# Kernel tuning notes

Hardware: AMD Instinct MI355X
Metric: run time of the kernel (lower is better)

The kernel has to match this reference:

```python
import jax, jax.numpy as jnp
import numpy as np

N, C, E = 4096, 128, 10          # nodes, channels, element types
LMAX = 2
NI = (LMAX + 1) ** 2             # 9 spherical components of node_feats
K = {1: 4, 2: 12, 3: 30}         # number of CG paths per correlation order
DIMS = [2 * L + 1 for L in range(LMAX + 1)]  # output irrep dims [1,3,5]


def setup_inputs() -> dict:
    key = jax.random.key(0)
    ks = iter(jax.random.split(key, 64))
    inp = {}
    inp["node_feats"] = jax.random.normal(next(ks), (N, C, NI), jnp.float32)
    inp["sc"] = jax.random.normal(next(ks), (N, C * sum(DIMS)), jnp.float32)
    z = jax.random.randint(next(ks), (N,), 0, E)
    inp["node_attrs"] = jax.nn.one_hot(z, E, dtype=jnp.float32)
    for L, d in enumerate(DIMS):
        # U tensors: fixed Clebsch-Gordan-structured constants (stand-in values,
        # correct shapes/contraction pattern of MACE's U_matrix buffers).
        inp[f"U3_L{L}"] = jax.random.normal(next(ks), (d, NI, NI, NI, K[3]), jnp.float32) * 0.05
        inp[f"U2_L{L}"] = jax.random.normal(next(ks), (d, NI, NI, K[2]), jnp.float32) * 0.05
        inp[f"U1_L{L}"] = jax.random.normal(next(ks), (d, NI, K[1]), jnp.float32) * 0.05
        # Element-dependent path weights [num_elements, k, channels]
        inp[f"W3_L{L}"] = jax.random.normal(next(ks), (E, K[3], C), jnp.float32) / np.sqrt(K[3])
        inp[f"W2_L{L}"] = jax.random.normal(next(ks), (E, K[2], C), jnp.float32) / np.sqrt(K[2])
        inp[f"W1_L{L}"] = jax.random.normal(next(ks), (E, K[1], C), jnp.float32) / np.sqrt(K[1])
        # o3.Linear channel-mixing weight for this irrep
        inp[f"lin_L{L}"] = jax.random.normal(next(ks), (C, C), jnp.float32)
    return inp


def _contract(x, y, U3, U2, U1, W3, W2, W1):
    """MACE symmetric contraction (correlation=3) for one output irrep.
    x: [b,c,n] node feats, y: [b,e] one-hot element attrs.
    Recursive einsum structure from mace.modules.symmetric_contraction.Contraction."""
    out = jnp.einsum('dijnk,ekc,bcn,be->bcdij', U3, W3, x, y)
    c2 = jnp.einsum('dijk,ekc,be->bcdij', U2, W2, y) + out
    out = jnp.einsum('bcdij,bcj->bcdi', c2, x)
    c1 = jnp.einsum('dik,ekc,be->bcdi', U1, W1, y) + out
    return jnp.einsum('bcdi,bci->bcd', c1, x)  # [b,c,d]


def reference(node_feats, sc, node_attrs,
              U3_L0, U2_L0, U1_L0, W3_L0, W2_L0, W1_L0, lin_L0,
              U3_L1, U2_L1, U1_L1, W3_L1, W2_L1, W1_L1, lin_L1,
              U3_L2, U2_L2, U1_L2, W3_L2, W2_L2, W1_L2, lin_L2):
    Us = [(U3_L0, U2_L0, U1_L0), (U3_L1, U2_L1, U1_L1), (U3_L2, U2_L2, U1_L2)]
    Ws = [(W3_L0, W2_L0, W1_L0), (W3_L1, W2_L1, W1_L1), (W3_L2, W2_L2, W1_L2)]
    lins = [lin_L0, lin_L1, lin_L2]
    c = node_feats.shape[1]
    norm = jnp.asarray(1.0 / np.sqrt(c), node_feats.dtype)
    outs = []
    for (u3, u2, u1), (w3, w2, w1), lw in zip(Us, Ws, lins):
        o = _contract(node_feats, node_attrs, u3, u2, u1, w3, w2, w1)  # [b,c,d]
        o = jnp.einsum('bcd,cf->bfd', o, lw) * norm                    # o3.Linear mix
        outs.append(o.reshape(o.shape[0], -1))
    return jnp.concatenate(outs, axis=-1) + sc
```

## Files before the change

kernel.cpp:

```cpp
#include <hip/hip_runtime.h>

#define NNODES 4096
#define NCH    128
#define NE     10
#define PADN   4736
#define NCHUNK 74
#define TSTRIDE 2048
#define DGSTRIDE 672


struct MTab { unsigned short v[220]; };
static constexpr MTab make_mtab() {
    MTab t{};
    int m = 0;
    for (int i = 0; i < 9; ++i) {
        t.v[m++] = (unsigned short)((1 << 12) | (i << 8) | (i << 4) | i);
        for (int j = i; j < 9; ++j) {
            t.v[m++] = (unsigned short)((2 << 12) | (i << 8) | (j << 4) | j);
            for (int n = j; n < 9; ++n)
                t.v[m++] = (unsigned short)((3 << 12) | (i << 8) | (j << 4) | n);
        }
    }
    return t;
}
__constant__ MTab c_mtab = make_mtab();

__device__ __forceinline__ float dot30(const float* __restrict__ U3, int dloc, int row,
                                       const float (&w3)[30])
{
    const float2* u = (const float2*)(U3 + ((size_t)dloc * 729 + row) * 30);
    float v = 0.0f;
#pragma unroll
    for (int kk = 0; kk < 15; ++kk) {
        float2 a = u[kk];
        v = fmaf(a.x, w3[2 * kk], v);
        v = fmaf(a.y, w3[2 * kk + 1], v);
    }
    return v;
}

__global__ __launch_bounds__(256) void k_pre(
    const float* __restrict__ attrs,
    const float* __restrict__ U3_0, const float* __restrict__ U3_1, const float* __restrict__ U3_2,
    const float* __restrict__ W3_0, const float* __restrict__ W3_1, const float* __restrict__ W3_2,
    const float* __restrict__ U2_0, const float* __restrict__ U2_1, const float* __restrict__ U2_2,
    const float* __restrict__ W2_0, const float* __restrict__ W2_1, const float* __restrict__ W2_2,
    const float* __restrict__ U1_0, const float* __restrict__ U1_1, const float* __restrict__ U1_2,
    const float* __restrict__ W1_0, const float* __restrict__ W1_1, const float* __restrict__ W1_2,
    float* __restrict__ Sws, int* __restrict__ list, int* __restrict__ chunkinfo)
{
    __shared__ __align__(16) float tile[32 * 129];
    int bid = blockIdx.x, t = threadIdx.x;
    if (bid < 630) {
        int e = bid / 63, r = bid - e * 63;
        int D = r / 7, chunk0 = (r - D * 7) * 32;
        int c = t & 127, sub = t >> 7;
        const float *U3, *U2, *U1, *W3, *W2, *W1; int dloc;
        if (D == 0)      { U3 = U3_0; U2 = U2_0; U1 = U1_0; W3 = W3_0; W2 = W2_0; W1 = W1_0; dloc = 0; }
        else if (D < 4)  { U3 = U3_1; U2 = U2_1; U1 = U1_1; W3 = W3_1; W2 = W2_1; W1 = W1_1; dloc = D - 1; }
        else             { U3 = U3_2; U2 = U2_2; U1 = U1_2; W3 = W3_2; W2 = W2_2; W1 = W1_2; dloc = D - 4; }
        float w3[30], w2[12], w1[4];
#pragma unroll
        for (int k = 0; k < 30; ++k) w3[k] = W3[((size_t)e * 30 + k) * 128 + c];
#pragma unroll
        for (int k = 0; k < 12; ++k) w2[k] = W2[((size_t)e * 12 + k) * 128 + c];
#pragma unroll
        for (int k = 0; k < 4; ++k)  w1[k] = W1[((size_t)e * 4 + k) * 128 + c];
#pragma unroll 1
        for (int rr = sub * 16; rr < sub * 16 + 16; ++rr) {
            int m = chunk0 + rr;
            float val = 0.0f;
            if (m < 219) {
                unsigned mv = c_mtab.v[m];
                int kind = mv >> 12, i = (mv >> 8) & 15, j = (mv >> 4) & 15, n = mv & 15;
                if (kind == 1) {
                    const float* u = U1 + (size_t)(dloc * 9 + i) * 4;
#pragma unroll
                    for (int k = 0; k < 4; ++k) val = fmaf(u[k], w1[k], val);
                } else if (kind == 2) {
                    const float* ua = U2 + (size_t)(dloc * 81 + i * 9 + j) * 12;
#pragma unroll
                    for (int k = 0; k < 12; ++k) val = fmaf(ua[k], w2[k], val);
                    if (i != j) {
                        const float* ub = U2 + (size_t)(dloc * 81 + j * 9 + i) * 12;
#pragma unroll
                        for (int k = 0; k < 12; ++k) val = fmaf(ub[k], w2[k], val);
                    }
                } else {
                    int r1 = -1, r2 = -1, r3 = -1, r4 = -1, r5 = -1;
                    if (i == j) {
                        if (j != n) { r1 = i * 81 + n * 9 + i; r2 = n * 81 + i * 9 + i; }
                    } else if (j == n) {
                        r1 = j * 81 + i * 9 + j; r2 = j * 81 + j * 9 + i;
                    } else {
                        r1 = i * 81 + n * 9 + j; r2 = j * 81 + i * 9 + n;
                        r3 = j * 81 + n * 9 + i; r4 = n * 81 + i * 9 + j;
                        r5 = n * 81 + j * 9 + i;
                    }
                    val = dot30(U3, dloc, i * 81 + j * 9 + n, w3);
                    if (r1 >= 0) { val += dot30(U3, dloc, r1, w3); val += dot30(U3, dloc, r2, w3); }
                    if (r3 >= 0) {
                        val += dot30(U3, dloc, r3, w3); val += dot30(U3, dloc, r4, w3);
                        val += dot30(U3, dloc, r5, w3);
                    }
                }
            }
            tile[rr * 129 + c] = val;
        }
        __syncthreads();
        int dg = D / 3, dr = D - dg * 3;
#pragma unroll 1
        for (int wv = 0; wv < 16; ++wv) {
            int idx = t + 256 * wv;
            int cc = idx >> 5, rr = idx & 31;
            int m = chunk0 + rr;
            if (m < 219)
                Sws[((size_t)e * 128 + cc) * TSTRIDE + dg * DGSTRIDE + m * 3 + dr] = tile[rr * 129 + cc];
        }
    } else {
        __shared__ int hist[NE], cur[NE], base[NE + 1], cbase[NE + 1];
        if (t < NE) { hist[t] = 0; cur[t] = 0; }
        __syncthreads();
        int mye[16];
#pragma unroll
        for (int k = 0; k < 16; ++k) {
            int b = k * 256 + t;
            const float* y = attrs + (size_t)b * NE;
            int e = 0;
#pragma unroll
            for (int u = 0; u < NE; ++u) if (y[u] > 0.5f) e = u;
            mye[k] = e;
            atomicAdd(&hist[e], 1);
        }
        for (int i = t; i < PADN; i += 256) list[i] = -1;
        __syncthreads();
        if (t == 0) {
            int off = 0, goff = 0;
            for (int e = 0; e < NE; ++e) {
                base[e] = off; cbase[e] = goff;
                int nc = (hist[e] + 63) >> 6;
                off += nc * 64; goff += nc;
            }
            base[NE] = off; cbase[NE] = goff;
        }
        __syncthreads();
        if (t < 80) {
            int info = -1;
            if (t < cbase[NE]) {
                int e = 0;
                while (!(t >= cbase[e] && t < cbase[e + 1])) ++e;
                int k = t - cbase[e];
                int valid = hist[e] - k * 64; if (valid > 64) valid = 64;
                info = (base[e] + k * 64) | (valid << 16) | (e << 24);
            }
            chunkinfo[t] = info;
        }
#pragma unroll
        for (int k = 0; k < 16; ++k) {
            int e = mye[k];
            int pos = atomicAdd(&cur[e], 1);
            list[base[e] + pos] = k * 256 + t;
        }
    }
}

__global__ __launch_bounds__(256) void k_gather(
    const float* __restrict__ nf, const int* __restrict__ list, float* __restrict__ xg)
{
    __shared__ __align__(16) float smem[64 * 73];
    __shared__ int lb[64];
    int qb = blockIdx.x >> 4, ct = blockIdx.x & 15;
    int c0 = ct * 8;
    int t = threadIdx.x;
    if (t < 64) lb[t] = list[qb * 64 + t];
    __syncthreads();
#pragma unroll 1
    for (int k = 0; k < 18; ++k) {
        int idx = k * 256 + t;
        int node = idx / 72, elem = idx - node * 72;
        int nb = lb[node];
        float v = 0.0f;
        if (nb >= 0) v = nf[(size_t)nb * 1152 + c0 * 9 + elem];
        smem[node * 73 + elem] = v;
    }
    __syncthreads();
#pragma unroll 1
    for (int k = 0; k < 18; ++k) {
        int idx = k * 256 + t;
        int node = idx & 63, re = idx >> 6;
        xg[((size_t)(c0 * 9 + re)) * PADN + qb * 64 + node] = smem[node * 73 + re];
    }
}

__global__ __launch_bounds__(256) void k_main(
    const float* __restrict__ xg, const int* __restrict__ chunkinfo,
    const float* __restrict__ Sws, float* __restrict__ pre)
{
    __shared__ __align__(16) float tabs[4][TSTRIDE];
    int c = blockIdx.x;
    int w = threadIdx.x >> 6, lane = threadIdx.x & 63;
    int g = blockIdx.y * 4 + w;
    int info = __builtin_amdgcn_readfirstlane(chunkinfo[g]);
    if (info == -1) return;
    int beg = info & 0xffff;
    int e = (info >> 24) & 0xff;
    int pos = beg + lane;

    {
        const float4* src = (const float4*)(Sws + ((size_t)e * NCH + c) * TSTRIDE);
        float4* dst = (float4*)tabs[w];
#pragma unroll
        for (int k = 0; k < 8; ++k)
            dst[lane + k * 64] = src[lane + k * 64];
    }

    const float* xq = xg + (size_t)c * 9 * PADN;
    float* prep     = pre + (size_t)c * 9 * PADN;

    float x[9];
#pragma unroll
    for (int n = 0; n < 9; ++n) x[n] = xq[(size_t)n * PADN + pos];

#pragma unroll 1
    for (int dg = 0; dg < 3; ++dg) {
        const float* s = tabs[w] + dg * DGSTRIDE;
        float a3[3] = {0.0f, 0.0f, 0.0f};
        int p = 0;
#pragma unroll
        for (int i = 0; i < 9; ++i) {
            float a2[3];
#pragma unroll
            for (int d = 0; d < 3; ++d) a2[d] = s[p + d];
            p += 3;
#pragma unroll
            for (int j = i; j < 9; ++j) {
                float a1[3];
#pragma unroll
                for (int d = 0; d < 3; ++d) a1[d] = s[p + d];
                p += 3;
#pragma unroll
                for (int n = j; n < 9; ++n) {
#pragma unroll
                    for (int d = 0; d < 3; ++d) a1[d] = fmaf(s[p + d], x[n], a1[d]);
                    p += 3;
                }
#pragma unroll
                for (int d = 0; d < 3; ++d) a2[d] = fmaf(a1[d], x[j], a2[d]);
            }
#pragma unroll
            for (int d = 0; d < 3; ++d) a3[d] = fmaf(a2[d], x[i], a3[d]);
        }
#pragma unroll
        for (int d = 0; d < 3; ++d)
            prep[(size_t)(dg * 3 + d) * PADN + pos] = a3[d];
    }
}

__global__ __launch_bounds__(256) void k_mixout(
    const float* __restrict__ pre, const int* __restrict__ list,
    const int* __restrict__ chunkinfo, const float* __restrict__ sc,
    const float* __restrict__ lin0, const float* __restrict__ lin1,
    const float* __restrict__ lin2, float* __restrict__ out)
{
    __shared__ __align__(16) float pt[128 * 64];
    int g = blockIdx.x, D = blockIdx.y;
    if (chunkinfo[g] == -1) return;
    int t = threadIdx.x;

    {
        int q4 = (t & 15) * 4;
        int cb = t >> 4;
#pragma unroll
        for (int k = 0; k < 8; ++k) {
            int c = cb + k * 16;
            float4 v = *(const float4*)&pre[((size_t)c * 9 + D) * PADN + g * 64 + q4];
            *(float4*)&pt[c * 64 + q4] = v;
        }
    }
    __syncthreads();

    int tq = t & 63;
    int f0 = __builtin_amdgcn_readfirstlane(t >> 6) * 32;
    int q = g * 64 + tq;
    const float* lin; int L, dl;
    if (D == 0)      { lin = lin0; L = 0; dl = 0; }
    else if (D < 4)  { lin = lin1; L = 1; dl = D - 1; }
    else             { lin = lin2; L = 2; dl = D - 4; }

    float acc[32];
#pragma unroll
    for (int f = 0; f < 32; ++f) acc[f] = 0.0f;

#pragma unroll 4
    for (int c = 0; c < 128; ++c) {
        float pv = pt[c * 64 + tq];
        const float* lr = lin + c * 128 + f0;
#pragma unroll
        for (int f = 0; f < 32; ++f)
            acc[f] = fmaf(pv, lr[f], acc[f]);
    }

    int b = list[q];
    if (b < 0) return;
    const float nrm = 0.08838834764831845f;
    const float* scb = sc + (size_t)b * 1152;
    float* ob = out + (size_t)b * 1152;
    if (L == 0) {
#pragma unroll
        for (int f = 0; f < 32; ++f)
            ob[f0 + f] = fmaf(nrm, acc[f], scb[f0 + f]);
    } else if (L == 1) {
#pragma unroll
        for (int f = 0; f < 32; ++f) {
            int col = 128 + (f0 + f) * 3 + dl;
            ob[col] = fmaf(nrm, acc[f], scb[col]);
        }
    } else {
#pragma unroll
        for (int f = 0; f < 32; ++f) {
            int col = 512 + (f0 + f) * 5 + dl;
            ob[col] = fmaf(nrm, acc[f], scb[col]);
        }
    }
}

extern "C" void kernel_launch(void* const* d_in, const int* in_sizes, int n_in,
                              void* d_out, int out_size, void* d_ws, size_t ws_size,
                              hipStream_t stream)
{
    const float* nf    = (const float*)d_in[0];
    const float* sc    = (const float*)d_in[1];
    const float* attrs = (const float*)d_in[2];
    const float *U3s[3], *U2s[3], *U1s[3], *W3s[3], *W2s[3], *W1s[3], *lins[3];
    for (int L = 0; L < 3; ++L) {
        const int o = 3 + 7 * L;
        U3s[L]  = (const float*)d_in[o + 0];
        U2s[L]  = (const float*)d_in[o + 1];
        U1s[L]  = (const float*)d_in[o + 2];
        W3s[L]  = (const float*)d_in[o + 3];
        W2s[L]  = (const float*)d_in[o + 4];
        W1s[L]  = (const float*)d_in[o + 5];
        lins[L] = (const float*)d_in[o + 6];
    }

    float* wsf     = (float*)d_ws;
    int* chunkinfo = (int*)d_ws;
    int* list      = chunkinfo + 80;
    float* Sws = wsf + 4864;
    float* pre = Sws + (size_t)NE * NCH * TSTRIDE;
    float* xg  = pre + (size_t)NCH * 9 * PADN;

    k_pre<<<631, 256, 0, stream>>>(attrs,
                                   U3s[0], U3s[1], U3s[2], W3s[0], W3s[1], W3s[2],
                                   U2s[0], U2s[1], U2s[2], W2s[0], W2s[1], W2s[2],
                                   U1s[0], U1s[1], U1s[2], W1s[0], W1s[1], W1s[2],
                                   Sws, list, chunkinfo);
    k_gather<<<1184, 256, 0, stream>>>(nf, list, xg);
    k_main<<<dim3(128, 19), 256, 0, stream>>>(xg, chunkinfo, Sws, pre);
    k_mixout<<<dim3(NCHUNK, 9), 256, 0, stream>>>(pre, list, chunkinfo, sc,
                                                  lins[0], lins[1], lins[2], (float*)d_out);
}
```

Measured before the change: 294.4 us.

## Split mix/output into two kernels with coalesced scatter; aggregate histogram atomics

Splits the fused channel-mix and output-scatter into two kernels. k_mix computes the linear mix into an intermediate buffer (reusing the gather workspace) with more blocks and fewer accumulators per thread. k_out then transposes tiles through shared memory so each node's output row is written contiguously with sc added, replacing the strided per-column global stores. The node-bucketing in k_pre also switches from one shared atomic per node to wave-level ballot aggregation. This adds an extra launch and a round trip through global memory for the mixed values.

New measurement: 435.0 us. 1.48x slower.

```diff
diff --git a/kernel.cpp b/kernel.cpp
--- a/kernel.cpp
+++ b/kernel.cpp
@@ -119,6 +119,8 @@
         }
     } else {
         __shared__ int hist[NE], cur[NE], base[NE + 1], cbase[NE + 1];
+        int lane = t & 63;
+        unsigned long long lmask = (1ull << lane) - 1ull;
         if (t < NE) { hist[t] = 0; cur[t] = 0; }
         __syncthreads();
         int mye[16];
@@ -130,7 +132,12 @@
 #pragma unroll
             for (int u = 0; u < NE; ++u) if (y[u] > 0.5f) e = u;
             mye[k] = e;
-            atomicAdd(&hist[e], 1);
+#pragma unroll
+            for (int u = 0; u < NE; ++u) {
+                unsigned long long m = __ballot(e == u);
+                if (m != 0ull && lane == (__ffsll((long long)m) - 1))
+                    atomicAdd(&hist[u], __popcll(m));
+            }
         }
         for (int i = t; i < PADN; i += 256) list[i] = -1;
         __syncthreads();
@@ -158,8 +165,18 @@
 #pragma unroll
         for (int k = 0; k < 16; ++k) {
             int e = mye[k];
-            int pos = atomicAdd(&cur[e], 1);
-            list[base[e] + pos] = k * 256 + t;
+#pragma unroll
+            for (int u = 0; u < NE; ++u) {
+                unsigned long long m = __ballot(e == u);
+                if (m != 0ull) {
+                    int leader = __ffsll((long long)m) - 1;
+                    int bs = 0;
+                    if (lane == leader) bs = atomicAdd(&cur[u], __popcll(m));
+                    bs = __shfl(bs, leader);
+                    if (e == u)
+                        list[base[u] + bs + __popcll(m & lmask)] = k * 256 + t;
+                }
+            }
         }
     }
 }
@@ -256,15 +273,20 @@
     }
 }
 
-__global__ __launch_bounds__(256) void k_mixout(
-    const float* __restrict__ pre, const int* __restrict__ list,
-    const int* __restrict__ chunkinfo, const float* __restrict__ sc,
+__global__ __launch_bounds__(256) void k_mix(
+    const float* __restrict__ pre, const int* __restrict__ chunkinfo,
     const float* __restrict__ lin0, const float* __restrict__ lin1,
-    const float* __restrict__ lin2, float* __restrict__ out)
+    const float* __restrict__ lin2, float* __restrict__ mixed)
 {
     __shared__ __align__(16) float pt[128 * 64];
-    int g = blockIdx.x, D = blockIdx.y;
+    int bid = blockIdx.x;
+    int nt = bid >> 1;
+    int fbase = (bid & 1) * 64;
+    int n0 = nt * 64;
+    int D = nt / NCHUNK;
+    int g = nt - D * NCHUNK;
     if (chunkinfo[g] == -1) return;
+    const float* lin = (D == 0) ? lin0 : (D < 4 ? lin1 : lin2);
     int t = threadIdx.x;
 
     {
@@ -273,54 +295,67 @@
 #pragma unroll
         for (int k = 0; k < 8; ++k) {
             int c = cb + k * 16;
-            float4 v = *(const float4*)&pre[((size_t)c * 9 + D) * PADN + g * 64 + q4];
+            float4 v = *(const float4*)&pre[(size_t)c * 9 * PADN + n0 + q4];
             *(float4*)&pt[c * 64 + q4] = v;
         }
     }
     __syncthreads();
 
     int tq = t & 63;
-    int f0 = __builtin_amdgcn_readfirstlane(t >> 6) * 32;
-    int q = g * 64 + tq;
-    const float* lin; int L, dl;
-    if (D == 0)      { lin = lin0; L = 0; dl = 0; }
-    else if (D < 4)  { lin = lin1; L = 1; dl = D - 1; }
-    else             { lin = lin2; L = 2; dl = D - 4; }
-
-    float acc[32];
-#pragma unroll
-    for (int f = 0; f < 32; ++f) acc[f] = 0.0f;
+    int f0 = fbase + __builtin_amdgcn_readfirstlane(t >> 6) * 16;
+    float acc[16];
+#pragma unroll
+    for (int f = 0; f < 16; ++f) acc[f] = 0.0f;
 
 #pragma unroll 4
     for (int c = 0; c < 128; ++c) {
         float pv = pt[c * 64 + tq];
         const float* lr = lin + c * 128 + f0;
 #pragma unroll
-        for (int f = 0; f < 32; ++f)
+        for (int f = 0; f < 16; ++f)
             acc[f] = fmaf(pv, lr[f], acc[f]);
     }
 
-    int b = list[q];
-    if (b < 0) return;
     const float nrm = 0.08838834764831845f;
-    const float* scb = sc + (size_t)b * 1152;
-    float* ob = out + (size_t)b * 1152;
-    if (L == 0) {
-#pragma unroll
-        for (int f = 0; f < 32; ++f)
-            ob[f0 + f] = fmaf(nrm, acc[f], scb[f0 + f]);
-    } else if (L == 1) {
-#pragma unroll
-        for (int f = 0; f < 32; ++f) {
-            int col = 128 + (f0 + f) * 3 + dl;
-            ob[col] = fmaf(nrm, acc[f], scb[col]);
-        }
-    } else {
-#pragma unroll
-        for (int f = 0; f < 32; ++f) {
-            int col = 512 + (f0 + f) * 5 + dl;
-            ob[col] = fmaf(nrm, acc[f], scb[col]);
-        }
+#pragma unroll
+    for (int f = 0; f < 16; ++f)
+        mixed[(size_t)(f0 + f) * 9 * PADN + n0 + tq] = acc[f] * nrm;
+}
+
+__global__ __launch_bounds__(256) void k_out(
+    const float* __restrict__ mixed, const int* __restrict__ list,
+    const int* __restrict__ chunkinfo, const float* __restrict__ sc,
+    float* __restrict__ out)
+{
+    __shared__ float tr[64 * 73];
+    int fc = blockIdx.x, g = blockIdx.y;
+    if (chunkinfo[g] == -1) return;
+    int t = threadIdx.x;
+    int fbase = fc * 8;
+    int tf = t >> 6, tq = t & 63;
+
+#pragma unroll
+    for (int k = 0; k < 18; ++k) {
+        int row = k * 4 + tf;
+        int f = row / 9, D = row - f * 9;
+        float v = mixed[((size_t)(fbase + f) * 9 + D) * PADN + g * 64 + tq];
+        tr[tq * 73 + row] = v;
+    }
+    __syncthreads();
+
+#pragma unroll 1
+    for (int k = 0; k < 18; ++k) {
+        int idx = k * 256 + t;
+        int node = idx / 72, col = idx - node * 72;
+        int b = list[g * 64 + node];
+        if (b < 0) continue;
+        int row, gcol;
+        if (col < 8)       { row = col * 9;                       gcol = fbase + col; }
+        else if (col < 32) { int u = col - 8;  int f = u / 3, dl = u - f * 3;
+                             row = f * 9 + 1 + dl;                gcol = 128 + fbase * 3 + u; }
+        else               { int u = col - 32; int f = u / 5, dl = u - f * 5;
+                             row = f * 9 + 4 + dl;                gcol = 512 + fbase * 5 + u; }
+        out[(size_t)b * 1152 + gcol] = tr[node * 73 + row] + sc[(size_t)b * 1152 + gcol];
     }
 }
 
@@ -349,6 +384,7 @@
     float* Sws = wsf + 4864;
     float* pre = Sws + (size_t)NE * NCH * TSTRIDE;
     float* xg  = pre + (size_t)NCH * 9 * PADN;
+    float* mixed = xg;
 
     k_pre<<<631, 256, 0, stream>>>(attrs,
                                    U3s[0], U3s[1], U3s[2], W3s[0], W3s[1], W3s[2],
@@ -357,6 +393,6 @@
                                    Sws, list, chunkinfo);
     k_gather<<<1184, 256, 0, stream>>>(nf, list, xg);
     k_main<<<dim3(128, 19), 256, 0, stream>>>(xg, chunkinfo, Sws, pre);
-    k_mixout<<<dim3(NCHUNK, 9), 256, 0, stream>>>(pre, list, chunkinfo, sc,
-                                                  lins[0], lins[1], lins[2], (float*)d_out);
-}
+    k_mix<<<1332, 256, 0, stream>>>(pre, chunkinfo, lins[0], lins[1], lins[2], mixed);
+    k_out<<<dim3(16, NCHUNK), 256, 0, stream>>>(mixed, list, chunkinfo, sc, (float*)d_out);
+}
```
